# Optimization experiments

Measured on AMD Instinct MI355X. Metric: run time of the kernel, lower is better.

Reference implementation:

```python
import jax, jax.numpy as jnp
import numpy as np

# ---- dims derived from Decoder(input_size=64, hidden_size=64, output_size=64, n_units=512) ----
B, L, I = 512, 256, 64
N_UNITS, N_MOTOR = 512, 64
N_COMMAND = max(int(0.4 * (N_UNITS - N_MOTOR)), 1)   # 179 (AutoNCP rule)
N_INTER = N_UNITS - N_MOTOR - N_COMMAND              # 269
SENSORY_FANOUT = max(int(N_INTER * 0.5), 1)          # density_level = 0.5
INTER_FANOUT = max(int(N_COMMAND * 0.5), 1)
MOTOR_FANIN = max(int(N_COMMAND * 0.5), 1)


def _make_masks():
    # Binary NCP connectivity (CfCCell uses abs(mask), so polarity is irrelevant).
    rng = np.random.RandomState(22222)
    m0 = np.zeros((I, N_INTER), np.float32)           # sensory -> inter
    for r in range(I):
        m0[r, rng.choice(N_INTER, SENSORY_FANOUT, replace=False)] = 1.0
    m1 = np.zeros((N_INTER, N_COMMAND), np.float32)   # inter -> command
    for r in range(N_INTER):
        m1[r, rng.choice(N_COMMAND, INTER_FANOUT, replace=False)] = 1.0
    m2 = np.zeros((N_COMMAND, N_MOTOR), np.float32)   # command -> motor (fanin per motor)
    for c in range(N_MOTOR):
        m2[rng.choice(N_COMMAND, MOTOR_FANIN, replace=False), c] = 1.0
    # WiredCfCCell: per-layer mask = [input_sparsity ; ones(h,h)]^T -> shape (h, in+h)
    def cellmask(m, h):
        return np.concatenate([m, np.ones((h, h), np.float32)], axis=0).T
    return (jnp.asarray(cellmask(m0, N_INTER)),
            jnp.asarray(cellmask(m1, N_COMMAND)),
            jnp.asarray(cellmask(m2, N_MOTOR)))


def _lin(key, out_f, in_f):
    kw, kb = jax.random.split(key)
    bound = 1.0 / np.sqrt(in_f)
    W = jax.random.uniform(kw, (out_f, in_f), jnp.float32, -bound, bound)
    b = jax.random.uniform(kb, (out_f,), jnp.float32, -bound, bound)
    return W, b


def setup_inputs() -> dict:
    key = jax.random.key(0)
    ks = jax.random.split(key, 8)
    dt = jax.random.uniform(ks[0], (B, L, I), jnp.float32)
    hidden_state = jax.random.normal(ks[1], (B, N_UNITS), jnp.float32) * 0.1
    M0, M1, M2 = _make_masks()
    # Each layer fuses ff1, ff2, time_a, time_b -> one (4h, in+h) weight.
    W0, b0 = _lin(ks[2], 4 * N_INTER, I + N_INTER)
    W1, b1 = _lin(ks[3], 4 * N_COMMAND, N_INTER + N_COMMAND)
    W2, b2 = _lin(ks[4], 4 * N_MOTOR, N_COMMAND + N_MOTOR)
    b0 = b0.reshape(4, N_INTER).reshape(-1)  # no-op, keeps layout explicit
    Wout, bout = _lin(ks[5], N_MOTOR, N_MOTOR)  # nn.Linear(hidden_size=64, output_size=64)
    return {"dt": dt, "hidden_state": hidden_state,
            "W0": W0, "b0": b0, "W1": W1, "b1": b1, "W2": W2, "b2": b2,
            "Wout": Wout, "bout": bout, "M0": M0, "M1": M1, "M2": M2}


def _masked_weight(W, M, h):
    # sparsity mask applies to ff1 and ff2 only; time_a/time_b stay dense
    return jnp.concatenate([W[:h] * M, W[h:2 * h] * M, W[2 * h:]], axis=0)


def _cell(x_in, h, Weff, b):
    # CfC 'default' mode, no backbone, ts = 1.0
    x = jnp.concatenate([x_in, h], axis=-1)
    z = x @ Weff.T + b
    ff1, ff2, ta, tb = jnp.split(z, 4, axis=-1)
    ti = jax.nn.sigmoid(ta * 1.0 + tb)
    return jnp.tanh(ff1) * (1.0 - ti) + ti * jnp.tanh(ff2)


def reference(dt, hidden_state, W0, b0, W1, b1, W2, b2, Wout, bout, M0, M1, M2):
    We0 = _masked_weight(W0, M0, N_INTER)
    We1 = _masked_weight(W1, M1, N_COMMAND)
    We2 = _masked_weight(W2, M2, N_MOTOR)
    h0 = hidden_state[:, :N_INTER]
    h1 = hidden_state[:, N_INTER:N_INTER + N_COMMAND]
    h2 = hidden_state[:, N_INTER + N_COMMAND:]

    def step(carry, x_t):
        a, b_, c = carry
        a = _cell(x_t, a, We0, b0)   # inter layer
        b_ = _cell(a, b_, We1, b1)   # command layer
        c = _cell(b_, c, We2, b2)    # motor layer (CfC output per step)
        return (a, b_, c), c

    _, ys = jax.lax.scan(step, (h0, h1, h2), jnp.swapaxes(dt, 0, 1))
    seq = jnp.swapaxes(ys, 0, 1)          # (B, L, N_MOTOR)
    return seq @ Wout.T + bout            # output_layer
```

## Files before the change

### kernel.cpp

```cpp
#include <hip/hip_runtime.h>
#include <stdint.h>

typedef _Float16 f16x8 __attribute__((ext_vector_type(8)));
typedef unsigned short u16x8 __attribute__((ext_vector_type(8)));
typedef float f32x4 __attribute__((ext_vector_type(4)));
typedef unsigned int u32x4 __attribute__((ext_vector_type(4)));

#define MFMA16(a,b,c) __builtin_amdgcn_mfma_f32_16x16x32_f16((a),(b),(c),0,0,0)

#define LSEQ 256
#define H0N  269
#define H1N  179
#define H0P  272
#define H1P  192
#define K0REAL 333
#define K1REAL 448
#define K2REAL 243
#define KK0  11
#define KK1  15
#define KK2  8
#define XH0S 360
#define XH1S 488
#define XH2S 200
#define MR   32

#define H0_OFF   0
#define H0_SLOT  (MR*H0P*2)
#define H1_OFF   (8*H0_SLOT)
#define H1_SLOT  (MR*H1P*2)
#define C2_OFF   (H1_OFF + 8*H1_SLOT)
#define CNT_OFF  (C2_OFF + 4096)
#define GSTRIDE  262144

#define BIGNEG   (-(1<<28))
#define NQ0 5
#define NQ1 8
#define NQ2 3

__device__ __forceinline__ unsigned short f2h_bits(float v) {
  return __builtin_bit_cast(unsigned short, (_Float16)v);
}
__device__ __forceinline__ float rcpf(float x) { return __builtin_amdgcn_rcpf(x); }
__device__ __forceinline__ float fast_sig(float s) { return rcpf(1.f + __expf(-s)); }
__device__ __forceinline__ float fast_tanh(float x) {
  float e = __expf(2.f * x);
  return 1.f - 2.f * rcpf(e + 1.f);
}

__device__ __forceinline__ u16x8 ldg16s(const unsigned short* p) {
  u16x8 r;
  asm volatile("global_load_dwordx4 %0, %1, off sc0 sc1" : "=v"(r) : "v"(p));
  return r;
}
__device__ __forceinline__ void stg16s(unsigned short* p, u16x8 v) {
  asm volatile("global_store_dwordx4 %0, %1, off sc0 sc1" :: "v"(p), "v"(v) : "memory");
}
__device__ __forceinline__ unsigned ld_flag(const unsigned int* p) {
  unsigned v;
  asm volatile("global_load_dword %0, %1, off sc0 sc1" : "=v"(v) : "v"(p) : "memory");
  return v;
}
__device__ __forceinline__ void st_flag(unsigned int* p, unsigned v) {
  asm volatile("global_store_dword %0, %1, off sc0 sc1" :: "v"(p), "v"(v) : "memory");
}
#define VM_WAIT0 do { asm volatile("s_waitcnt vmcnt(0)" ::: "memory"); __builtin_amdgcn_sched_barrier(0); } while (0)

__device__ __forceinline__ bool chunk_fresh(u16x8 v, unsigned tp) {
  u32x4 d = __builtin_bit_cast(u32x4, v);
  return ((d[0] & 0x00010001u) == tp) & ((d[1] & 0x00010001u) == tp) &
         ((d[2] & 0x00010001u) == tp) & ((d[3] & 0x00010001u) == tp);
}
__device__ __forceinline__ u16x8 tag_chunk(u16x8 v, unsigned tp) {
  u32x4 d = __builtin_bit_cast(u32x4, v);
  d &= 0xFFFEFFFEu;
  d |= tp;
  return __builtin_bit_cast(u16x8, d);
}

__global__ void __launch_bounds__(256) init_state(const float* __restrict__ hs, char* __restrict__ ws) {
  int g = blockIdx.x, tid = threadIdx.x;
  char* gb = ws + (size_t)g * GSTRIDE;
  uint4 z4 = {0,0,0,0};
  int total16 = (CNT_OFF + 512) / 16;
  for (int i = tid; i < total16; i += 256) ((uint4*)gb)[i] = z4;
  __syncthreads();
  int b0 = g * MR;
  unsigned short* H0 = (unsigned short*)(gb + H0_OFF + 7*(size_t)H0_SLOT);
  unsigned short* H1 = (unsigned short*)(gb + H1_OFF + 7*(size_t)H1_SLOT);
  unsigned short* C2 = (unsigned short*)(gb + C2_OFF);
  for (int i = tid; i < MR*H0P; i += 256) { int r = i/H0P, c = i%H0P;
    H0[i] = (c < H0N) ? (unsigned short)(f2h_bits(hs[(size_t)(b0+r)*512 + c]) & 0xFFFEu) : (unsigned short)0; }
  for (int i = tid; i < MR*H1P; i += 256) { int r = i/H1P, c = i%H1P;
    H1[i] = (c < H1N) ? (unsigned short)(f2h_bits(hs[(size_t)(b0+r)*512 + H0N + c]) & 0xFFFEu) : (unsigned short)0; }
  for (int i = tid; i < MR*64;  i += 256) { int r = i>>6,  c = i&63;
    C2[i] = f2h_bits(hs[(size_t)(b0+r)*512 + 448 + c]); }
}

template<int KK, int MODE>
__device__ __forceinline__ void build_frag3(f16x8* wf, const float* __restrict__ W, const float* __restrict__ Msk,
                                            int h, int Kreal, int g4, int tile, int lane) {
  int col = tile * 16 + (lane & 15);
  bool nv = (col < h);
  #pragma unroll
  for (int kk = 0; kk < KK; ++kk) {
    f16x8 s;
    #pragma unroll
    for (int e = 0; e < 8; ++e) {
      int k = kk*32 + ((lane >> 4) << 3) + e;
      int wc;
      if (MODE == 0)      wc = (k < 333) ? k : -1;
      else if (MODE == 1) wc = (k < 269) ? k : ((k >= 272 && k < 451) ? (k - 3) : -1);
      else                wc = (k < 179) ? k : ((k >= 192 && k < 256) ? (k - 13) : -1);
      float val = 0.f;
      if (nv && wc >= 0) {
        if (g4 < 2) val = W[(size_t)(g4 * h + col) * Kreal + wc] * Msk[(size_t)col * Kreal + wc];
        else        val = W[(size_t)(2 * h + col) * Kreal + wc] + W[(size_t)(3 * h + col) * Kreal + wc];
      }
      s[e] = (_Float16)val;
    }
    wf[kk] = s;
  }
}

__device__ __forceinline__ f16x8 lda(const unsigned short* xh, int stride, int mt, int kk, int lane) {
  const unsigned short* p = xh + (size_t)(mt*16 + (lane & 15)) * stride + kk*32 + ((lane >> 4) << 3);
  return __builtin_bit_cast(f16x8, *(const u16x8*)p);
}

__global__ void __launch_bounds__(256, 1) rnn_persist(
    const float* __restrict__ dt,
    const float* __restrict__ W0, const float* __restrict__ b0v,
    const float* __restrict__ W1, const float* __restrict__ b1v,
    const float* __restrict__ W2, const float* __restrict__ b2v,
    const float* __restrict__ Wout, const float* __restrict__ boutg,
    const float* __restrict__ M0, const float* __restrict__ M1, const float* __restrict__ M2,
    float* __restrict__ out, char* __restrict__ ws)
{
  __shared__ __attribute__((aligned(16))) unsigned short xhS[MR * XH1S];
  __shared__ __attribute__((aligned(16))) unsigned short hbuf[4][32][16];

  int tid = threadIdx.x;
  int lane = tid & 63, wave = tid >> 6;
  int bid = blockIdx.x;
  int j = bid >> 4;
  int g = bid & 15;
  int b0 = g * MR;

  char* gb = ws + (size_t)g * GSTRIDE;
  unsigned short* H0r = (unsigned short*)(gb + H0_OFF);
  unsigned short* H1r = (unsigned short*)(gb + H1_OFF);
  unsigned int*   cnt = (unsigned int*)(gb + CNT_OFF);
  u16x8 zz = {0,0,0,0,0,0,0,0};

  if (j < 5) {
    int tile = j*4 + wave;
    bool act = (tile < 17);
    int ncol = tile*16 + (lane & 15);
    bool cok = act && (ncol < H0N);
    f16x8 wf[3][KK0];
    if (act) {
      #pragma unroll
      for (int g4 = 0; g4 < 3; ++g4) build_frag3<KK0,0>(wf[g4], W0, M0, H0N, K0REAL, g4, tile, lane);
    }
    float bb[3] = {0.f,0.f,0.f};
    if (cok) {
      bb[0] = b0v[ncol]; bb[1] = b0v[H0N + ncol];
      bb[2] = b0v[2*H0N + ncol] + b0v[3*H0N + ncol];
    }
    if (tid < 64) {
      int r = tid >> 1, c8 = 336 + (tid & 1)*8;
      *(u16x8*)(xhS + (size_t)r*XH0S + c8) = zz;
    }
    int aoff[NQ0], adst[NQ0]; bool aval[NQ0];
    #pragma unroll
    for (int q = 0; q < NQ0; ++q) {
      int idx = tid + q*256;
      aval[q] = (idx < MR*34);
      int r = idx / 34, cc = (idx % 34) * 8;
      aoff[q] = r*H0P + cc;
      adst[q] = r*XH0S + 64 + cc;
    }
    int xrow = tid >> 3, xc = (tid & 7) * 8;
    const float* dtb = dt + ((size_t)(b0 + xrow) * LSEQ) * 64 + xc;
    float4 xA = *(const float4*)(dtb);
    float4 xB = *(const float4*)(dtb + 4);
    int goff = (lane < 5) ? -6 : (lane < 8) ? -7 : BIGNEG;
    for (int t = 0; t < LSEQ; ++t) {
      unsigned tpm1 = (((unsigned)(t + 7) >> 3) & 1) * 0x00010001u;
      unsigned tpt  = (((unsigned)(t + 8) >> 3) & 1) * 0x00010001u;
      {
        unsigned short* d = xhS + (size_t)xrow*XH0S + xc;
        d[0]=f2h_bits(xA.x); d[1]=f2h_bits(xA.y); d[2]=f2h_bits(xA.z); d[3]=f2h_bits(xA.w);
        d[4]=f2h_bits(xB.x); d[5]=f2h_bits(xB.y); d[6]=f2h_bits(xB.z); d[7]=f2h_bits(xB.w);
      }
      const unsigned short* H0s = H0r + (size_t)((t + 7) & 7) * (MR*H0P);
      u16x8 tA[NQ0];
      for (int it = 0; it < (1 << 17); ++it) {
        unsigned gv = 0;
        if (lane < 8) gv = ld_flag(cnt + lane);
        #pragma unroll
        for (int q = 0; q < NQ0; ++q) if (aval[q]) tA[q] = ldg16s(H0s + aoff[q]);
        VM_WAIT0;
        bool ok = ((int)gv >= t + goff);
        #pragma unroll
        for (int q = 0; q < NQ0; ++q) if (aval[q]) ok &= chunk_fresh(tA[q], tpm1);
        if (__all(ok)) break;
        __builtin_amdgcn_s_sleep(1);
      }
      #pragma unroll
      for (int q = 0; q < NQ0; ++q) if (aval[q]) *(u16x8*)(xhS + adst[q]) = tA[q];
      __syncthreads();
      if (tid == 0) st_flag(&cnt[j], t + 1);
      { int tn = (t + 1 < LSEQ) ? t + 1 : t;
        xA = *(const float4*)(dtb + (size_t)tn*64);
        xB = *(const float4*)(dtb + (size_t)tn*64 + 4); }
      f32x4 ac[3][2];
      if (act) {
        #pragma unroll
        for (int g4 = 0; g4 < 3; ++g4) { ac[g4][0] = (f32x4){0,0,0,0}; ac[g4][1] = (f32x4){0,0,0,0}; }
        #pragma unroll
        for (int kk = 0; kk < KK0; ++kk) {
          f16x8 a0 = lda(xhS, XH0S, 0, kk, lane);
          f16x8 a1 = lda(xhS, XH0S, 1, kk, lane);
          #pragma unroll
          for (int g4 = 0; g4 < 3; ++g4) {
            ac[g4][0] = MFMA16(a0, wf[g4][kk], ac[g4][0]);
            ac[g4][1] = MFMA16(a1, wf[g4][kk], ac[g4][1]);
          }
        }
      }
      __syncthreads();
      if (act) {
        #pragma unroll
        for (int m = 0; m < 2; ++m) {
          #pragma unroll
          for (int r = 0; r < 4; ++r) {
            float ti = fast_sig(ac[2][m][r] + bb[2]);
            float hv = cok ? (fast_tanh(ac[0][m][r] + bb[0])*(1.f - ti) + ti*fast_tanh(ac[1][m][r] + bb[1])) : 0.f;
            hbuf[wave][m*16 + (lane>>4)*4 + r][lane & 15] = f2h_bits(hv);
          }
        }
        int row = lane >> 1, c8v = (lane & 1) * 8;
        u16x8 hv8 = tag_chunk(*(const u16x8*)&hbuf[wave][row][c8v], tpt);
        unsigned short* Hn = H0r + (size_t)(t & 7) * (MR*H0P);
        stg16s(Hn + (size_t)row*H0P + tile*16 + c8v, hv8);
      }
    }
  } else if (j < 8) {
    int tile = (j - 5)*4 + wave;
    int ncol = tile*16 + (lane & 15);
    bool cok = (ncol < H1N);
    f16x8 wf[3][KK1];
    #pragma unroll
    for (int g4 = 0; g4 < 3; ++g4) build_frag3<KK1,1>(wf[g4], W1, M1, H1N, K1REAL, g4, tile, lane);
    float bb[3] = {0.f,0.f,0.f};
    if (cok) {
      bb[0] = b1v[ncol]; bb[1] = b1v[H1N + ncol];
      bb[2] = b1v[2*H1N + ncol] + b1v[3*H1N + ncol];
    }
    if (tid < 64) {
      int r = tid >> 1, c8 = 464 + (tid & 1)*8;
      *(u16x8*)(xhS + (size_t)r*XH1S + c8) = zz;
    }
    int soff[NQ1], sdst[NQ1]; bool sval[NQ1], sisB[NQ1];
    #pragma unroll
    for (int q = 0; q < NQ1; ++q) {
      int idx = tid + q*256;
      if (idx < 1088) {
        sval[q] = true; sisB[q] = false;
        int r = idx / 34, cc = (idx % 34) * 8;
        soff[q] = r*H0P + cc; sdst[q] = r*XH1S + cc;
      } else {
        int i2 = idx - 1088;
        sval[q] = (i2 < 768); sisB[q] = true;
        int r = i2 / 24, cc = (i2 % 24) * 8;
        soff[q] = r*H1P + cc; sdst[q] = r*XH1S + 272 + cc;
      }
    }
    int goff = (lane >= 5 && lane < 8) ? -6 : (lane == 8) ? -7 : BIGNEG;
    for (int t = 0; t < LSEQ; ++t) {
      unsigned tpm1 = (((unsigned)(t + 7) >> 3) & 1) * 0x00010001u;
      unsigned tpt  = (((unsigned)(t + 8) >> 3) & 1) * 0x00010001u;
      const unsigned short* As = H0r + (size_t)(t & 7) * (MR*H0P);
      const unsigned short* Bs = H1r + (size_t)((t + 7) & 7) * (MR*H1P);
      u16x8 tS[NQ1];
      for (int it = 0; it < (1 << 17); ++it) {
        unsigned gv = 0;
        if (lane >= 5 && lane < 9) gv = ld_flag(cnt + lane);
        #pragma unroll
        for (int q = 0; q < NQ1; ++q) if (sval[q]) tS[q] = ldg16s((sisB[q] ? Bs : As) + soff[q]);
        VM_WAIT0;
        bool ok = ((int)gv >= t + goff);
        #pragma unroll
        for (int q = 0; q < NQ1; ++q) if (sval[q]) ok &= chunk_fresh(tS[q], sisB[q] ? tpm1 : tpt);
        if (__all(ok)) break;
        __builtin_amdgcn_s_sleep(1);
      }
      #pragma unroll
      for (int q = 0; q < NQ1; ++q) if (sval[q]) *(u16x8*)(xhS + sdst[q]) = tS[q];
      __syncthreads();
      if (tid == 0) st_flag(&cnt[j], t + 1);
      f32x4 ac[3][2];
      #pragma unroll
      for (int g4 = 0; g4 < 3; ++g4) { ac[g4][0] = (f32x4){0,0,0,0}; ac[g4][1] = (f32x4){0,0,0,0}; }
      #pragma unroll
      for (int kk = 0; kk < KK1; ++kk) {
        f16x8 a0 = lda(xhS, XH1S, 0, kk, lane);
        f16x8 a1 = lda(xhS, XH1S, 1, kk, lane);
        #pragma unroll
        for (int g4 = 0; g4 < 3; ++g4) {
          ac[g4][0] = MFMA16(a0, wf[g4][kk], ac[g4][0]);
          ac[g4][1] = MFMA16(a1, wf[g4][kk], ac[g4][1]);
        }
      }
      __syncthreads();
      {
        #pragma unroll
        for (int m = 0; m < 2; ++m) {
          #pragma unroll
          for (int r = 0; r < 4; ++r) {
            float ti = fast_sig(ac[2][m][r] + bb[2]);
            float hv = cok ? (fast_tanh(ac[0][m][r] + bb[0])*(1.f - ti) + ti*fast_tanh(ac[1][m][r] + bb[1])) : 0.f;
            hbuf[wave][m*16 + (lane>>4)*4 + r][lane & 15] = f2h_bits(hv);
          }
        }
        int row = lane >> 1, c8v = (lane & 1) * 8;
        u16x8 hv8 = tag_chunk(*(const u16x8*)&hbuf[wave][row][c8v], tpt);
        unsigned short* Hn = H1r + (size_t)(t & 7) * (MR*H1P);
        stg16s(Hn + (size_t)row*H1P + tile*16 + c8v, hv8);
      }
    }
  } else {
    int tile = wave;
    int ncol = tile*16 + (lane & 15);
    f16x8 wf[3][KK2], woutf[2];
    #pragma unroll
    for (int g4 = 0; g4 < 3; ++g4) build_frag3<KK2,2>(wf[g4], W2, M2, 64, K2REAL, g4, tile, lane);
    {
      #pragma unroll
      for (int kk = 0; kk < 2; ++kk) {
        f16x8 s;
        #pragma unroll
        for (int e = 0; e < 8; ++e) {
          int k = kk*32 + ((lane >> 4) << 3) + e;
          s[e] = (_Float16)Wout[(size_t)ncol*64 + k];
        }
        woutf[kk] = s;
      }
    }
    float bov = boutg[ncol];
    float bb[3];
    bb[0] = b2v[ncol]; bb[1] = b2v[64 + ncol];
    bb[2] = b2v[2*64 + ncol] + b2v[3*64 + ncol];
    {
      const unsigned short* C2i = (const unsigned short*)(gb + C2_OFF);
      int r = tid >> 3, c8 = (tid & 7) * 8;
      u16x8 cv = ldg16s(C2i + r*64 + c8);
      VM_WAIT0;
      *(u16x8*)&hbuf[c8 >> 4][r][c8 & 15] = cv;
    }
    int soff[NQ2], sdst[NQ2];
    #pragma unroll
    for (int q = 0; q < NQ2; ++q) {
      int idx = tid + q*256;
      int r = idx / 24, cc = (idx % 24) * 8;
      soff[q] = r*H1P + cc; sdst[q] = r*XH2S + cc;
    }
    for (int t = 0; t < LSEQ; ++t) {
      unsigned tpt = (((unsigned)(t + 8) >> 3) & 1) * 0x00010001u;
      const unsigned short* Bs = H1r + (size_t)(t & 7) * (MR*H1P);
      u16x8 tS[NQ2];
      for (int it = 0; it < (1 << 17); ++it) {
        #pragma unroll
        for (int q = 0; q < NQ2; ++q) tS[q] = ldg16s(Bs + soff[q]);
        VM_WAIT0;
        bool ok = true;
        #pragma unroll
        for (int q = 0; q < NQ2; ++q) ok &= chunk_fresh(tS[q], tpt);
        if (__all(ok)) break;
        __builtin_amdgcn_s_sleep(1);
      }
      #pragma unroll
      for (int q = 0; q < NQ2; ++q) *(u16x8*)(xhS + sdst[q]) = tS[q];
      __syncthreads();
      if (tid == 0) st_flag(&cnt[8], t + 1);
      f32x4 ac[3][2];
      #pragma unroll
      for (int g4 = 0; g4 < 3; ++g4) { ac[g4][0] = (f32x4){0,0,0,0}; ac[g4][1] = (f32x4){0,0,0,0}; }
      #pragma unroll
      for (int kk = 0; kk < KK2; ++kk) {
        f16x8 a0, a1;
        if (kk < 6) {
          a0 = lda(xhS, XH2S, 0, kk, lane);
          a1 = lda(xhS, XH2S, 1, kk, lane);
        } else {
          int k0 = kk*32 + ((lane >> 4) << 3) - 192;
          a0 = __builtin_bit_cast(f16x8, *(const u16x8*)&hbuf[k0 >> 4][(lane & 15)][k0 & 15]);
          a1 = __builtin_bit_cast(f16x8, *(const u16x8*)&hbuf[k0 >> 4][16 + (lane & 15)][k0 & 15]);
        }
        #pragma unroll
        for (int g4 = 0; g4 < 3; ++g4) {
          ac[g4][0] = MFMA16(a0, wf[g4][kk], ac[g4][0]);
          ac[g4][1] = MFMA16(a1, wf[g4][kk], ac[g4][1]);
        }
      }
      __syncthreads();
      {
        #pragma unroll
        for (int m = 0; m < 2; ++m) {
          #pragma unroll
          for (int r = 0; r < 4; ++r) {
            float ti = fast_sig(ac[2][m][r] + bb[2]);
            float hv = fast_tanh(ac[0][m][r] + bb[0])*(1.f - ti) + ti*fast_tanh(ac[1][m][r] + bb[1]);
            hbuf[wave][m*16 + (lane>>4)*4 + r][lane & 15] = f2h_bits(hv);
          }
        }
      }
      __syncthreads();
      {
        #pragma unroll
        for (int m = 0; m < 2; ++m) {
          f32x4 acc = {0.f,0.f,0.f,0.f};
          #pragma unroll
          for (int kk = 0; kk < 2; ++kk) {
            int k0 = kk*32 + ((lane >> 4) << 3);
            f16x8 a = __builtin_bit_cast(f16x8, *(const u16x8*)&hbuf[k0 >> 4][m*16 + (lane & 15)][k0 & 15]);
            acc = MFMA16(a, woutf[kk], acc);
          }
          int cc = lane & 15, rb = (lane >> 4) * 4;
          #pragma unroll
          for (int r = 0; r < 4; ++r) {
            int row = m*16 + rb + r;
            out[((size_t)(b0 + row) * LSEQ + t) * 64 + tile*16 + cc] = acc[r] + bov;
          }
        }
      }
    }
  }
}

extern "C" void kernel_launch(void* const* d_in, const int* in_sizes, int n_in,
                              void* d_out, int out_size, void* d_ws, size_t ws_size,
                              hipStream_t stream) {
  const float* dt   = (const float*)d_in[0];
  const float* hs   = (const float*)d_in[1];
  const float* W0   = (const float*)d_in[2];
  const float* b0v  = (const float*)d_in[3];
  const float* W1   = (const float*)d_in[4];
  const float* b1v  = (const float*)d_in[5];
  const float* W2   = (const float*)d_in[6];
  const float* b2v  = (const float*)d_in[7];
  const float* Wo   = (const float*)d_in[8];
  const float* bo   = (const float*)d_in[9];
  const float* M0   = (const float*)d_in[10];
  const float* M1   = (const float*)d_in[11];
  const float* M2   = (const float*)d_in[12];
  (void)in_sizes; (void)n_in; (void)out_size; (void)ws_size;
  init_state<<<16, 256, 0, stream>>>(hs, (char*)d_ws);
  rnn_persist<<<144, 256, 0, stream>>>(dt, W0, b0v, W1, b1v, W2, b2v, Wo, bo, M0, M1, M2,
                                       (float*)d_out, (char*)d_ws);
}
```

Measured before the change: 1.064 ms.

## Double-buffer the LDS input tile to drop a per-step barrier, spin before sleeping

The shared xh staging buffer now has two copies that alternate by timestep parity. Each step's writes therefore cannot clobber data other waves are still reading from the previous step, so the second __syncthreads per step is removed in the inter and command layer loops. The polling loops also spin without s_sleep for the first few iterations, which should shorten wake-up latency at the cost of more memory polling. LDS use doubles, and the motor branch keeps its barriers.

```diff
diff --git a/kernel.cpp b/kernel.cpp
--- a/kernel.cpp
+++ b/kernel.cpp
@@ -136,8 +136,8 @@
     const float* __restrict__ M0, const float* __restrict__ M1, const float* __restrict__ M2,
     float* __restrict__ out, char* __restrict__ ws)
 {
-  __shared__ __attribute__((aligned(16))) unsigned short xhS[MR * XH1S];
-  __shared__ __attribute__((aligned(16))) unsigned short hbuf[4][32][16];
+  __shared__ __attribute__((aligned(16))) unsigned short xhS[2][MR * XH1S];
+  __shared__ __attribute__((aligned(16))) unsigned short hbuf[4][MR][16];
 
   int tid = threadIdx.x;
   int lane = tid & 63, wave = tid >> 6;
@@ -150,12 +150,13 @@
   unsigned short* H0r = (unsigned short*)(gb + H0_OFF);
   unsigned short* H1r = (unsigned short*)(gb + H1_OFF);
   unsigned int*   cnt = (unsigned int*)(gb + CNT_OFF);
+  int r0 = lane & 15;
   u16x8 zz = {0,0,0,0,0,0,0,0};
 
   if (j < 5) {
     int tile = j*4 + wave;
     bool act = (tile < 17);
-    int ncol = tile*16 + (lane & 15);
+    int ncol = tile*16 + r0;
     bool cok = act && (ncol < H0N);
     f16x8 wf[3][KK0];
     if (act) {
@@ -167,9 +168,9 @@
       bb[0] = b0v[ncol]; bb[1] = b0v[H0N + ncol];
       bb[2] = b0v[2*H0N + ncol] + b0v[3*H0N + ncol];
     }
-    if (tid < 64) {
-      int r = tid >> 1, c8 = 336 + (tid & 1)*8;
-      *(u16x8*)(xhS + (size_t)r*XH0S + c8) = zz;
+    if (tid < 128) {
+      int r = (tid & 63) >> 1, c8 = 336 + (tid & 1)*8;
+      *(u16x8*)(&xhS[tid >> 6][(size_t)r*XH0S + c8]) = zz;
     }
     int aoff[NQ0], adst[NQ0]; bool aval[NQ0];
     #pragma unroll
@@ -185,11 +186,13 @@
     float4 xA = *(const float4*)(dtb);
     float4 xB = *(const float4*)(dtb + 4);
     int goff = (lane < 5) ? -6 : (lane < 8) ? -7 : BIGNEG;
+    __syncthreads();
     for (int t = 0; t < LSEQ; ++t) {
+      unsigned short* xb = xhS[t & 1];
       unsigned tpm1 = (((unsigned)(t + 7) >> 3) & 1) * 0x00010001u;
       unsigned tpt  = (((unsigned)(t + 8) >> 3) & 1) * 0x00010001u;
       {
-        unsigned short* d = xhS + (size_t)xrow*XH0S + xc;
+        unsigned short* d = xb + (size_t)xrow*XH0S + xc;
         d[0]=f2h_bits(xA.x); d[1]=f2h_bits(xA.y); d[2]=f2h_bits(xA.z); d[3]=f2h_bits(xA.w);
         d[4]=f2h_bits(xB.x); d[5]=f2h_bits(xB.y); d[6]=f2h_bits(xB.z); d[7]=f2h_bits(xB.w);
       }
@@ -205,10 +208,10 @@
         #pragma unroll
         for (int q = 0; q < NQ0; ++q) if (aval[q]) ok &= chunk_fresh(tA[q], tpm1);
         if (__all(ok)) break;
-        __builtin_amdgcn_s_sleep(1);
-      }
-      #pragma unroll
-      for (int q = 0; q < NQ0; ++q) if (aval[q]) *(u16x8*)(xhS + adst[q]) = tA[q];
+        if (it >= 4) __builtin_amdgcn_s_sleep(1);
+      }
+      #pragma unroll
+      for (int q = 0; q < NQ0; ++q) if (aval[q]) *(u16x8*)(xb + adst[q]) = tA[q];
       __syncthreads();
       if (tid == 0) st_flag(&cnt[j], t + 1);
       { int tn = (t + 1 < LSEQ) ? t + 1 : t;
@@ -220,35 +223,32 @@
         for (int g4 = 0; g4 < 3; ++g4) { ac[g4][0] = (f32x4){0,0,0,0}; ac[g4][1] = (f32x4){0,0,0,0}; }
         #pragma unroll
         for (int kk = 0; kk < KK0; ++kk) {
-          f16x8 a0 = lda(xhS, XH0S, 0, kk, lane);
-          f16x8 a1 = lda(xhS, XH0S, 1, kk, lane);
+          f16x8 a0 = lda(xb, XH0S, 0, kk, lane);
+          f16x8 a1 = lda(xb, XH0S, 1, kk, lane);
           #pragma unroll
           for (int g4 = 0; g4 < 3; ++g4) {
             ac[g4][0] = MFMA16(a0, wf[g4][kk], ac[g4][0]);
             ac[g4][1] = MFMA16(a1, wf[g4][kk], ac[g4][1]);
           }
         }
-      }
-      __syncthreads();
-      if (act) {
         #pragma unroll
         for (int m = 0; m < 2; ++m) {
           #pragma unroll
           for (int r = 0; r < 4; ++r) {
             float ti = fast_sig(ac[2][m][r] + bb[2]);
             float hv = cok ? (fast_tanh(ac[0][m][r] + bb[0])*(1.f - ti) + ti*fast_tanh(ac[1][m][r] + bb[1])) : 0.f;
-            hbuf[wave][m*16 + (lane>>4)*4 + r][lane & 15] = f2h_bits(hv);
+            hbuf[wave][m*16 + (lane>>4)*4 + r][r0] = f2h_bits(hv);
           }
         }
-        int row = lane >> 1, c8v = (lane & 1) * 8;
-        u16x8 hv8 = tag_chunk(*(const u16x8*)&hbuf[wave][row][c8v], tpt);
+        int srow = lane >> 1, c8v = (lane & 1) * 8;
+        u16x8 hv8 = tag_chunk(*(const u16x8*)&hbuf[wave][srow][c8v], tpt);
         unsigned short* Hn = H0r + (size_t)(t & 7) * (MR*H0P);
-        stg16s(Hn + (size_t)row*H0P + tile*16 + c8v, hv8);
+        stg16s(Hn + (size_t)srow*H0P + tile*16 + c8v, hv8);
       }
     }
   } else if (j < 8) {
     int tile = (j - 5)*4 + wave;
-    int ncol = tile*16 + (lane & 15);
+    int ncol = tile*16 + r0;
     bool cok = (ncol < H1N);
     f16x8 wf[3][KK1];
     #pragma unroll
@@ -258,9 +258,9 @@
       bb[0] = b1v[ncol]; bb[1] = b1v[H1N + ncol];
       bb[2] = b1v[2*H1N + ncol] + b1v[3*H1N + ncol];
     }
-    if (tid < 64) {
-      int r = tid >> 1, c8 = 464 + (tid & 1)*8;
-      *(u16x8*)(xhS + (size_t)r*XH1S + c8) = zz;
+    if (tid < 128) {
+      int r = (tid & 63) >> 1, c8 = 464 + (tid & 1)*8;
+      *(u16x8*)(&xhS[tid >> 6][(size_t)r*XH1S + c8]) = zz;
     }
     int soff[NQ1], sdst[NQ1]; bool sval[NQ1], sisB[NQ1];
     #pragma unroll
@@ -278,7 +278,9 @@
       }
     }
     int goff = (lane >= 5 && lane < 8) ? -6 : (lane == 8) ? -7 : BIGNEG;
+    __syncthreads();
     for (int t = 0; t < LSEQ; ++t) {
+      unsigned short* xb = xhS[t & 1];
       unsigned tpm1 = (((unsigned)(t + 7) >> 3) & 1) * 0x00010001u;
       unsigned tpt  = (((unsigned)(t + 8) >> 3) & 1) * 0x00010001u;
       const unsigned short* As = H0r + (size_t)(t & 7) * (MR*H0P);
@@ -292,12 +294,14 @@
         VM_WAIT0;
         bool ok = ((int)gv >= t + goff);
         #pragma unroll
-        for (int q = 0; q < NQ1; ++q) if (sval[q]) ok &= chunk_fresh(tS[q], sisB[q] ? tpm1 : tpt);
+        for (int q = 0; q < NQ1; ++q) {
+          if (sval[q]) ok &= chunk_fresh(tS[q], sisB[q] ? tpm1 : tpt);
+        }
         if (__all(ok)) break;
-        __builtin_amdgcn_s_sleep(1);
-      }
-      #pragma unroll
-      for (int q = 0; q < NQ1; ++q) if (sval[q]) *(u16x8*)(xhS + sdst[q]) = tS[q];
+        if (it >= 4) __builtin_amdgcn_s_sleep(1);
+      }
+      #pragma unroll
+      for (int q = 0; q < NQ1; ++q) if (sval[q]) *(u16x8*)(xb + sdst[q]) = tS[q];
       __syncthreads();
       if (tid == 0) st_flag(&cnt[j], t + 1);
       f32x4 ac[3][2];
@@ -305,34 +309,32 @@
       for (int g4 = 0; g4 < 3; ++g4) { ac[g4][0] = (f32x4){0,0,0,0}; ac[g4][1] = (f32x4){0,0,0,0}; }
       #pragma unroll
       for (int kk = 0; kk < KK1; ++kk) {
-        f16x8 a0 = lda(xhS, XH1S, 0, kk, lane);
-        f16x8 a1 = lda(xhS, XH1S, 1, kk, lane);
+        f16x8 a0 = lda(xb, XH1S, 0, kk, lane);
+        f16x8 a1 = lda(xb, XH1S, 1, kk, lane);
         #pragma unroll
         for (int g4 = 0; g4 < 3; ++g4) {
           ac[g4][0] = MFMA16(a0, wf[g4][kk], ac[g4][0]);
           ac[g4][1] = MFMA16(a1, wf[g4][kk], ac[g4][1]);
         }
       }
-      __syncthreads();
-      {
-        #pragma unroll
-        for (int m = 0; m < 2; ++m) {
-          #pragma unroll
-          for (int r = 0; r < 4; ++r) {
-            float ti = fast_sig(ac[2][m][r] + bb[2]);
-            float hv = cok ? (fast_tanh(ac[0][m][r] + bb[0])*(1.f - ti) + ti*fast_tanh(ac[1][m][r] + bb[1])) : 0.f;
-            hbuf[wave][m*16 + (lane>>4)*4 + r][lane & 15] = f2h_bits(hv);
-          }
-        }
-        int row = lane >> 1, c8v = (lane & 1) * 8;
-        u16x8 hv8 = tag_chunk(*(const u16x8*)&hbuf[wave][row][c8v], tpt);
-        unsigned short* Hn = H1r + (size_t)(t & 7) * (MR*H1P);
-        stg16s(Hn + (size_t)row*H1P + tile*16 + c8v, hv8);
-      }
+      #pragma unroll
+      for (int m = 0; m < 2; ++m) {
+        #pragma unroll
+        for (int r = 0; r < 4; ++r) {
+          float ti = fast_sig(ac[2][m][r] + bb[2]);
+          float hv = cok ? (fast_tanh(ac[0][m][r] + bb[0])*(1.f - ti) + ti*fast_tanh(ac[1][m][r] + bb[1])) : 0.f;
+          hbuf[wave][m*16 + (lane>>4)*4 + r][r0] = f2h_bits(hv);
+        }
+      }
+      int srow = lane >> 1, c8v = (lane & 1) * 8;
+      u16x8 hv8 = tag_chunk(*(const u16x8*)&hbuf[wave][srow][c8v], tpt);
+      unsigned short* Hn = H1r + (size_t)(t & 7) * (MR*H1P);
+      stg16s(Hn + (size_t)srow*H1P + tile*16 + c8v, hv8);
     }
   } else {
     int tile = wave;
-    int ncol = tile*16 + (lane & 15);
+    int ncol = tile*16 + r0;
+    int ks = (lane >> 4) * 8;
     f16x8 wf[3][KK2], woutf[2];
     #pragma unroll
     for (int g4 = 0; g4 < 3; ++g4) build_frag3<KK2,2>(wf[g4], W2, M2, 64, K2REAL, g4, tile, lane);
@@ -342,7 +344,7 @@
         f16x8 s;
         #pragma unroll
         for (int e = 0; e < 8; ++e) {
-          int k = kk*32 + ((lane >> 4) << 3) + e;
+          int k = kk*32 + ks + e;
           s[e] = (_Float16)Wout[(size_t)ncol*64 + k];
         }
         woutf[kk] = s;
@@ -367,6 +369,7 @@
       soff[q] = r*H1P + cc; sdst[q] = r*XH2S + cc;
     }
     for (int t = 0; t < LSEQ; ++t) {
+      unsigned short* xb = xhS[t & 1];
       unsigned tpt = (((unsigned)(t + 8) >> 3) & 1) * 0x00010001u;
       const unsigned short* Bs = H1r + (size_t)(t & 7) * (MR*H1P);
       u16x8 tS[NQ2];
@@ -378,10 +381,10 @@
         #pragma unroll
         for (int q = 0; q < NQ2; ++q) ok &= chunk_fresh(tS[q], tpt);
         if (__all(ok)) break;
-        __builtin_amdgcn_s_sleep(1);
-      }
-      #pragma unroll
-      for (int q = 0; q < NQ2; ++q) *(u16x8*)(xhS + sdst[q]) = tS[q];
+        if (it >= 4) __builtin_amdgcn_s_sleep(1);
+      }
+      #pragma unroll
+      for (int q = 0; q < NQ2; ++q) *(u16x8*)(xb + sdst[q]) = tS[q];
       __syncthreads();
       if (tid == 0) st_flag(&cnt[8], t + 1);
       f32x4 ac[3][2];
@@ -391,12 +394,12 @@
       for (int kk = 0; kk < KK2; ++kk) {
         f16x8 a0, a1;
         if (kk < 6) {
-          a0 = lda(xhS, XH2S, 0, kk, lane);
-          a1 = lda(xhS, XH2S, 1, kk, lane);
+          a0 = lda(xb, XH2S, 0, kk, lane);
+          a1 = lda(xb, XH2S, 1, kk, lane);
         } else {
-          int k0 = kk*32 + ((lane >> 4) << 3) - 192;
-          a0 = __builtin_bit_cast(f16x8, *(const u16x8*)&hbuf[k0 >> 4][(lane & 15)][k0 & 15]);
-          a1 = __builtin_bit_cast(f16x8, *(const u16x8*)&hbuf[k0 >> 4][16 + (lane & 15)][k0 & 15]);
+          int k0 = kk*32 + ks - 192;
+          a0 = __builtin_bit_cast(f16x8, *(const u16x8*)&hbuf[k0 >> 4][r0][k0 & 15]);
+          a1 = __builtin_bit_cast(f16x8, *(const u16x8*)&hbuf[k0 >> 4][16 + r0][k0 & 15]);
         }
         #pragma unroll
         for (int g4 = 0; g4 < 3; ++g4) {
@@ -412,7 +415,7 @@
           for (int r = 0; r < 4; ++r) {
             float ti = fast_sig(ac[2][m][r] + bb[2]);
             float hv = fast_tanh(ac[0][m][r] + bb[0])*(1.f - ti) + ti*fast_tanh(ac[1][m][r] + bb[1]);
-            hbuf[wave][m*16 + (lane>>4)*4 + r][lane & 15] = f2h_bits(hv);
+            hbuf[wave][m*16 + (lane>>4)*4 + r][r0] = f2h_bits(hv);
           }
         }
       }
@@ -423,15 +426,15 @@
           f32x4 acc = {0.f,0.f,0.f,0.f};
           #pragma unroll
           for (int kk = 0; kk < 2; ++kk) {
-            int k0 = kk*32 + ((lane >> 4) << 3);
-            f16x8 a = __builtin_bit_cast(f16x8, *(const u16x8*)&hbuf[k0 >> 4][m*16 + (lane & 15)][k0 & 15]);
+            int k0 = kk*32 + ks;
+            f16x8 a = __builtin_bit_cast(f16x8, *(const u16x8*)&hbuf[k0 >> 4][m*16 + r0][k0 & 15]);
             acc = MFMA16(a, woutf[kk], acc);
           }
-          int cc = lane & 15, rb = (lane >> 4) * 4;
+          int rb = (lane >> 4) * 4;
           #pragma unroll
           for (int r = 0; r < 4; ++r) {
             int row = m*16 + rb + r;
-            out[((size_t)(b0 + row) * LSEQ + t) * 64 + tile*16 + cc] = acc[r] + bov;
+            out[((size_t)(b0 + row) * LSEQ + t) * 64 + tile*16 + r0] = acc[r] + bov;
           }
         }
       }
```

After: 1.038 ms. -2.5%, faster.
